# Kernel optimization log

Hardware: AMD Instinct MI355X
Metric: run time of the kernel (lower is better)

The kernel has to match this reference:

```python
import jax, jax.numpy as jnp
import numpy as np

B, N, DIM, H = 4, 2048, 1024, 8
HD = DIM // H
SCALE = HD ** -0.5


def setup_inputs() -> dict:
    key = jax.random.key(0)
    ks = jax.random.split(key, 9)
    inp = {
        "q": jax.random.normal(ks[0], (B, N, DIM), dtype=jnp.float32),
        "k": jax.random.normal(ks[1], (B, N, DIM), dtype=jnp.float32),
        "v": jax.random.normal(ks[2], (B, N, DIM), dtype=jnp.float32),
        "trans_mat": jax.random.normal(ks[3], (B, N, N), dtype=jnp.float32),
        # torch Linear weights: [out_features, in_features]; qkv_bias=False
        "Wq": jax.random.normal(ks[4], (DIM, DIM), dtype=jnp.float32) * (DIM ** -0.5),
        "Wk": jax.random.normal(ks[5], (DIM, DIM), dtype=jnp.float32) * (DIM ** -0.5),
        "Wv": jax.random.normal(ks[6], (DIM, DIM), dtype=jnp.float32) * (DIM ** -0.5),
        "Wp": jax.random.normal(ks[7], (DIM, DIM), dtype=jnp.float32) * (DIM ** -0.5),
        "bp": jax.random.normal(ks[8], (DIM,), dtype=jnp.float32) * 0.01,
    }
    return inp


def reference(q, k, v, trans_mat, Wq, Wk, Wv, Wp, bp):
    Bq, Nq, C = q.shape
    # project and split heads: [B, H, N, HD]
    qh = (q @ Wq.T).reshape(Bq, Nq, H, HD).transpose(0, 2, 1, 3)
    kh = (k @ Wk.T).reshape(Bq, -1, H, HD).transpose(0, 2, 1, 3)
    vh = (v @ Wv.T).reshape(Bq, -1, H, HD).transpose(0, 2, 1, 3)
    # scaled scores gated elementwise by trans_mat (broadcast over heads)
    scores = jnp.einsum("bhqd,bhkd->bhqk", qh, kh) * SCALE
    gated = scores * trans_mat[:, None, :, :]
    # softmax over full row, then zero out positions where gated == 0
    sm = jax.nn.softmax(gated, axis=-1)
    attn = jnp.where(gated != 0, sm, jnp.zeros((), dtype=sm.dtype))
    x = jnp.einsum("bhqk,bhkd->bhqd", attn, vh)
    x = x.transpose(0, 2, 1, 3).reshape(Bq, Nq, C)
    return x @ Wp.T + bp
```

## Files before the change

### kernel.cpp

```cpp
#include <hip/hip_runtime.h>
#include <hip/hip_bf16.h>
#include <stdint.h>

#define B_    4
#define N_    2048
#define DIM_  1024
#define H_    8
#define HD_   128
#define MTOK  (B_ * N_)
#define SCALE_  0.08838834764831845f
#define LOG2E_  1.4426950408889634f
#define QSCALE_ (SCALE_ * LOG2E_)

typedef unsigned short u16;
typedef __attribute__((ext_vector_type(4)))  float f32x4;
typedef __attribute__((ext_vector_type(16))) float f32x16;
typedef __attribute__((ext_vector_type(8)))  short s16x8;
typedef __attribute__((ext_vector_type(8)))  u16  u16x8;
typedef __attribute__((ext_vector_type(4)))  u16  u16x4;
typedef __attribute__((ext_vector_type(4)))  unsigned u32x4;

__device__ __forceinline__ u16 f2bf(float f) {
    uint32_t i = __builtin_bit_cast(uint32_t, f);
    return (u16)((i + 0x7FFFu + ((i >> 16) & 1u)) >> 16);
}
__device__ __forceinline__ unsigned pk_bf16(float a, float b) {
    unsigned r;
    asm("v_cvt_pk_bf16_f32 %0, %1, %2" : "=v"(r) : "v"(a), "v"(b));
    return r;
}
__device__ __forceinline__ void pl32_swap(unsigned &a, unsigned &b) {
    asm volatile("v_permlane32_swap_b32 %0, %1" : "+v"(a), "+v"(b));
}
__device__ __forceinline__ void gl_lds16(const u16* g, u16* l) {
    __builtin_amdgcn_global_load_lds((const __attribute__((address_space(1))) void*)g,
                                     (__attribute__((address_space(3))) void*)l,
                                     16, 0, 0);
}

__global__ __launch_bounds__(256) void cvt_f32_bf16(const float* __restrict__ src,
                                                    u16* __restrict__ dst, int n) {
    int i = (blockIdx.x * 256 + threadIdx.x) * 4;
    int stride = gridDim.x * 256 * 4;
    for (; i < n; i += stride) {
        float4 v = *(const float4*)(src + i);
        u16x4 o;
        o.x = f2bf(v.x); o.y = f2bf(v.y); o.z = f2bf(v.z); o.w = f2bf(v.w);
        *(u16x4*)(dst + i) = o;
    }
}

__global__ __launch_bounds__(256) void cvt_w4(const float* __restrict__ s0,
                                              const float* __restrict__ s1,
                                              const float* __restrict__ s2,
                                              const float* __restrict__ s3,
                                              u16* __restrict__ dst) {
    const float* s = blockIdx.y == 0 ? s0 : blockIdx.y == 1 ? s1 : blockIdx.y == 2 ? s2 : s3;
    u16* d = dst + (size_t)blockIdx.y * (DIM_ * DIM_);
    int i = (blockIdx.x * 256 + threadIdx.x) * 8;
    float4 a = *(const float4*)(s + i);
    float4 b = *(const float4*)(s + i + 4);
    u32x4 w = {pk_bf16(a.x, a.y), pk_bf16(a.z, a.w), pk_bf16(b.x, b.y), pk_bf16(b.z, b.w)};
    *(u16x8*)(d + i) = __builtin_bit_cast(u16x8, w);
}

__global__ __launch_bounds__(256) void transpose_f32(const float* __restrict__ in,
                                                     float* __restrict__ out) {
    __shared__ float t[64][65];
    const int r0 = blockIdx.y * 64, c0 = blockIdx.x * 64;
    const float* ib = in + (size_t)blockIdx.z * N_ * N_;
    float* ob = out + (size_t)blockIdx.z * N_ * N_;
    const int lr = threadIdx.x >> 6, lc = threadIdx.x & 63;
    #pragma unroll
    for (int i = 0; i < 16; i++)
        t[i * 4 + lr][lc] = ib[(size_t)(r0 + i * 4 + lr) * N_ + c0 + lc];
    __syncthreads();
    #pragma unroll
    for (int i = 0; i < 16; i++)
        ob[(size_t)(c0 + i * 4 + lr) * N_ + r0 + lc] = t[lc][i * 4 + lr];
}

template <int MODE>
__global__ __launch_bounds__(256) void gemm_bt(const u16* __restrict__ A,
                                               const u16* __restrict__ Bt,
                                               void* __restrict__ Cout,
                                               const float* __restrict__ bias,
                                               float scale, int M, int NN, int K) {
    __shared__ __align__(16) u16 lga[128 * 64];
    __shared__ __align__(16) u16 lgb[128 * 64];
    const int tid  = threadIdx.x;
    const int lane = tid & 63, wave = tid >> 6;
    const int wm = wave >> 1, wn = wave & 1;
    const int row0 = blockIdx.y * 128, col0 = blockIdx.x * 128;

    f32x4 acc[4][4] = {};

    auto stageLds = [&](const u16* G, u16* L, int rowbase, int k0) {
        #pragma unroll
        for (int i = 0; i < 4; i++) {
            int rb = wave * 32 + i * 8;
            int r  = rb + (lane >> 3);
            int cc = (lane & 7) ^ (lane >> 3);
            gl_lds16(G + (size_t)(rowbase + r) * K + k0 + cc * 8, L + rb * 64);
        }
    };

    for (int k0 = 0; k0 < K; k0 += 64) {
        stageLds(A,  lga, row0, k0);
        stageLds(Bt, lgb, col0, k0);
        __syncthreads();
        #pragma unroll
        for (int kk = 0; kk < 2; kk++) {
            s16x8 af[4], bfr[4];
            #pragma unroll
            for (int mi = 0; mi < 4; mi++) {
                int r = wm * 64 + mi * 16 + (lane & 15);
                int sc = (kk * 4 + (lane >> 4)) ^ (lane & 7);
                af[mi] = *(const s16x8*)(&lga[r * 64 + sc * 8]);
            }
            #pragma unroll
            for (int ni = 0; ni < 4; ni++) {
                int r = wn * 64 + ni * 16 + (lane & 15);
                int sc = (kk * 4 + (lane >> 4)) ^ (lane & 7);
                bfr[ni] = *(const s16x8*)(&lgb[r * 64 + sc * 8]);
            }
            #pragma unroll
            for (int mi = 0; mi < 4; mi++)
                #pragma unroll
                for (int ni = 0; ni < 4; ni++)
                    acc[mi][ni] = __builtin_amdgcn_mfma_f32_16x16x32_bf16(
                        af[mi], bfr[ni], acc[mi][ni], 0, 0, 0);
        }
        __syncthreads();
    }

    #pragma unroll
    for (int mi = 0; mi < 4; mi++) {
        #pragma unroll
        for (int ni = 0; ni < 4; ni++) {
            #pragma unroll
            for (int r = 0; r < 4; r++) {
                int grow = row0 + wm * 64 + mi * 16 + ((lane >> 4) << 2) + r;
                int gcol = col0 + wn * 64 + ni * 16 + (lane & 15);
                float vv = acc[mi][ni][r];
                if (MODE == 2) {
                    ((float*)Cout)[(size_t)grow * NN + gcol] = vv + bias[gcol];
                } else {
                    vv *= scale;
                    int bb = grow >> 11, n = grow & (N_ - 1);
                    int hh = gcol >> 7,  d = gcol & (HD_ - 1);
                    size_t idx = (MODE == 0)
                        ? ((size_t)(bb * H_ + hh) * N_ + n) * HD_ + d
                        : ((size_t)(bb * H_ + hh) * HD_ + d) * N_ + n;
                    ((u16*)Cout)[idx] = f2bf(vv);
                }
            }
        }
    }
}

__global__ __launch_bounds__(256, 2) void attn_swapped(const u16* __restrict__ Qh,
                                                       const u16* __restrict__ Kh,
                                                       const u16* __restrict__ Vt,
                                                       const float* __restrict__ transT,
                                                       u16* __restrict__ xout) {
    __shared__ __align__(16) u16 kt[2][64 * 128];
    __shared__ __align__(16) u16 vt[2][128 * 64];

    const int tid = threadIdx.x, lane = tid & 63, wave = tid >> 6;
    const int lq = lane & 31, hl = lane >> 5;

    int lin = blockIdx.x + 16 * (blockIdx.y + 8 * blockIdx.z);
    int nl  = (lin & 7) * 64 + (lin >> 3);
    const int qt = nl & 15, hh = (nl >> 4) & 7, b = nl >> 7;
    const int q0 = qt * 128 + wave * 32;
    const int q  = q0 + lq;

    const u16* Qbh = Qh + (size_t)(b * H_ + hh) * N_ * HD_;
    const u16* Kbh = Kh + (size_t)(b * H_ + hh) * N_ * HD_;
    const u16* Vbh = Vt + (size_t)(b * H_ + hh) * HD_ * N_;
    const float* tTq = transT + (size_t)b * N_ * N_ + q;

    s16x8 qf[8];
    #pragma unroll
    for (int s = 0; s < 8; s++)
        qf[s] = *(const s16x8*)(Qbh + (size_t)q * HD_ + s * 16 + hl * 8);

    auto stageKV = [&](int kv0, int bi) {
        #pragma unroll
        for (int i = 0; i < 4; i++) {
            int rk = wave * 16 + i * 4 + (lane >> 4);
            int ck = (lane & 15) ^ (rk & 15) ^ ((rk & 16) >> 2);
            gl_lds16(Kbh + (size_t)(kv0 + rk) * HD_ + ck * 8,
                     &kt[bi][(wave * 16 + i * 4) * 128]);
            int rv = wave * 32 + i * 8 + (lane >> 3);
            int cv = (lane & 7) ^ (rv & 7) ^ ((rv >> 3) & 3);
            gl_lds16(Vbh + (size_t)rv * N_ + kv0 + cv * 8,
                     &vt[bi][(wave * 32 + i * 8) * 64]);
        }
    };

    const int mKl = (lq & 15) ^ ((lq & 16) >> 2);
    const int mVl = (lq & 7) ^ ((lq >> 3) & 3);

    float m = -3.0e38f, l = 0.f;
    f32x16 aoT[4] = {};

    stageKV(0, 0);
    __syncthreads();

    for (int it = 0; it < N_ / 64; it++) {
        const int kv0 = it * 64, cur = it & 1;
        if (it + 1 < N_ / 64) stageKV(kv0 + 64, cur ^ 1);

        float tt[2][16];
        #pragma unroll
        for (int ni = 0; ni < 2; ni++)
            #pragma unroll
            for (int idx = 0; idx < 16; idx++) {
                int kv = (idx & 3) + 8 * (idx >> 2) + 4 * hl + 32 * ni;
                tt[ni][idx] = tTq[(size_t)(kv0 + kv) * N_];
            }

        f32x16 sT[2] = {};
        __builtin_amdgcn_s_setprio(1);
        #pragma unroll
        for (int s = 0; s < 8; s++)
            #pragma unroll
            for (int ni = 0; ni < 2; ni++) {
                int r = ni * 32 + lq;
                int slot = (2 * s + hl) ^ mKl;
                s16x8 kf = *(const s16x8*)(&kt[cur][r * 128 + slot * 8]);
                sT[ni] = __builtin_amdgcn_mfma_f32_32x32x16_bf16(kf, qf[s], sT[ni], 0, 0, 0);
            }
        __builtin_amdgcn_s_setprio(0);

        float mx = -3.0e38f;
        #pragma unroll
        for (int ni = 0; ni < 2; ni++)
            #pragma unroll
            for (int idx = 0; idx < 16; idx++) {
                float g = sT[ni][idx] * tt[ni][idx];
                sT[ni][idx] = g;
                mx = fmaxf(mx, g);
            }
        mx = fmaxf(mx, __shfl_xor(mx, 32));

        if (__any(mx > m + 8.0f)) {
            float mn = fmaxf(m, mx);
            float sfv = __builtin_amdgcn_exp2f(m - mn);
            m = mn;
            l *= sfv;
            #pragma unroll
            for (int dt = 0; dt < 4; dt++)
                #pragma unroll
                for (int e = 0; e < 16; e++) aoT[dt][e] *= sfv;
        }

        float rs = 0.f;
        #pragma unroll
        for (int ni = 0; ni < 2; ni++)
            #pragma unroll
            for (int e = 0; e < 16; e++) {
                float g = sT[ni][e];
                float p = __builtin_amdgcn_exp2f(g - m);
                rs += p;
                sT[ni][e] = (g != 0.0f) ? p : 0.0f;
            }
        rs += __shfl_xor(rs, 32);
        l += rs;

        s16x8 pfrag[4];
        #pragma unroll
        for (int sp = 0; sp < 4; sp++) {
            const int ni = sp >> 1;
            const int ru = (2 * sp) & 3, rv2 = (2 * sp + 1) & 3;
            unsigned u0 = pk_bf16(sT[ni][ru * 4 + 0], sT[ni][ru * 4 + 1]);
            unsigned u1 = pk_bf16(sT[ni][ru * 4 + 2], sT[ni][ru * 4 + 3]);
            unsigned v0 = pk_bf16(sT[ni][rv2 * 4 + 0], sT[ni][rv2 * 4 + 1]);
            unsigned v1 = pk_bf16(sT[ni][rv2 * 4 + 2], sT[ni][rv2 * 4 + 3]);
            pl32_swap(u0, v0);
            pl32_swap(u1, v1);
            u32x4 w = {u0, u1, v0, v1};
            pfrag[sp] = __builtin_bit_cast(s16x8, w);
        }

        __builtin_amdgcn_s_setprio(1);
        #pragma unroll
        for (int dt = 0; dt < 4; dt++)
            #pragma unroll
            for (int sp = 0; sp < 4; sp++) {
                int r = dt * 32 + lq;
                int slot = (2 * sp + hl) ^ mVl;
                s16x8 vf = *(const s16x8*)(&vt[cur][r * 64 + slot * 8]);
                aoT[dt] = __builtin_amdgcn_mfma_f32_32x32x16_bf16(vf, pfrag[sp], aoT[dt], 0, 0, 0);
            }
        __builtin_amdgcn_s_setprio(0);
        __syncthreads();
    }

    float inv = 1.0f / l;
    u16* orow = xout + ((size_t)(b * N_ + q)) * DIM_ + hh * HD_;
    #pragma unroll
    for (int dt = 0; dt < 4; dt++)
        #pragma unroll
        for (int r2 = 0; r2 < 4; r2++) {
            u16x4 ov;
            #pragma unroll
            for (int e = 0; e < 4; e++)
                ov[e] = f2bf(aoT[dt][r2 * 4 + e] * inv);
            *(u16x4*)(orow + dt * 32 + r2 * 8 + hl * 4) = ov;
        }
}

__global__ __launch_bounds__(512) void attn_fb(const u16* __restrict__ Qh,
                                               const u16* __restrict__ Kh,
                                               const u16* __restrict__ Vt,
                                               const float* __restrict__ trans,
                                               u16* __restrict__ xout) {
    __shared__ __align__(16) u16 kt[64 * 128];
    __shared__ __align__(16) u16 vt[128 * 64];
    __shared__ __align__(16) u16 plds[8][16 * 72];

    const int tid = threadIdx.x, lane = tid & 63, wave = tid >> 6;
    const int qt = blockIdx.x, h = blockIdx.y, b = blockIdx.z;
    const int qrow_base = qt * 128 + wave * 16;

    const u16* Qbh = Qh + (size_t)(b * H_ + h) * N_ * HD_;
    const u16* Kbh = Kh + (size_t)(b * H_ + h) * N_ * HD_;
    const u16* Vbh = Vt + (size_t)(b * H_ + h) * HD_ * N_;
    const float* trow = trans + (size_t)b * N_ * N_
                      + (size_t)(qrow_base + ((lane >> 4) << 2)) * N_ + (lane & 15);

    s16x8 qf[4];
    {
        int r = qrow_base + (lane & 15);
        #pragma unroll
        for (int kd = 0; kd < 4; kd++)
            qf[kd] = *(const s16x8*)(Qbh + (size_t)r * HD_ + kd * 32 + ((lane >> 4) << 3));
    }
    auto stageKV = [&](int kv0) {
        int rbk = wave * 8, rbv = wave * 16;
        #pragma unroll
        for (int j = 0; j < 2; j++) {
            int c = j * 64 + lane;
            int rk = rbk + (c >> 4), ck = (c & 15) ^ (rk & 15);
            gl_lds16(Kbh + (size_t)(kv0 + rk) * HD_ + ck * 8, kt + rbk * 128 + j * 512);
            int rv = rbv + (c >> 3), cv = (c & 7) ^ (rv & 7);
            gl_lds16(Vbh + (size_t)rv * N_ + kv0 + cv * 8, vt + rbv * 64 + j * 512);
        }
    };

    float m[4], l[4];
    #pragma unroll
    for (int r = 0; r < 4; r++) { m[r] = -3.0e38f; l[r] = 0.f; }
    f32x4 ao[8] = {};

    for (int kv0 = 0; kv0 < N_; kv0 += 64) {
        stageKV(kv0);
        __syncthreads();
        f32x4 s[4] = {};
        #pragma unroll
        for (int kd = 0; kd < 4; kd++)
            #pragma unroll
            for (int ni = 0; ni < 4; ni++) {
                int r = ni * 16 + (lane & 15);
                int sc = (kd * 4 + (lane >> 4)) ^ (lane & 15);
                s16x8 bfr = *(const s16x8*)(&kt[r * 128 + sc * 8]);
                s[ni] = __builtin_amdgcn_mfma_f32_16x16x32_bf16(qf[kd], bfr, s[ni], 0, 0, 0);
            }
        float pmax[4] = {-3.0e38f, -3.0e38f, -3.0e38f, -3.0e38f};
        #pragma unroll
        for (int ni = 0; ni < 4; ni++)
            #pragma unroll
            for (int r = 0; r < 4; r++) {
                float tt = trow[(size_t)r * N_ + kv0 + ni * 16];
                float gg = s[ni][r] * tt;
                s[ni][r] = gg;
                pmax[r] = fmaxf(pmax[r], gg);
            }
        #pragma unroll
        for (int r = 0; r < 4; r++) {
            float p = pmax[r];
            p = fmaxf(p, __shfl_xor(p, 1));
            p = fmaxf(p, __shfl_xor(p, 2));
            p = fmaxf(p, __shfl_xor(p, 4));
            p = fmaxf(p, __shfl_xor(p, 8));
            pmax[r] = p;
        }
        bool need = false;
        #pragma unroll
        for (int r = 0; r < 4; r++) need = need || (pmax[r] > m[r] + 8.0f);
        if (__any(need)) {
            #pragma unroll
            for (int r = 0; r < 4; r++) {
                float mn = fmaxf(m[r], pmax[r]);
                float sfv = __builtin_amdgcn_exp2f(m[r] - mn);
                m[r] = mn; l[r] *= sfv;
                #pragma unroll
                for (int t = 0; t < 8; t++) ao[t][r] *= sfv;
            }
        }
        float rowsum[4] = {0.f, 0.f, 0.f, 0.f};
        u16* pw = &plds[wave][0];
        #pragma unroll
        for (int ni = 0; ni < 4; ni++)
            #pragma unroll
            for (int r = 0; r < 4; r++) {
                float gg = s[ni][r];
                float e = __builtin_amdgcn_exp2f(gg - m[r]);
                rowsum[r] += e;
                float pe = (gg != 0.0f) ? e : 0.0f;
                pw[(((lane >> 4) << 2) + r) * 72 + ni * 16 + (lane & 15)] = f2bf(pe);
            }
        #pragma unroll
        for (int r = 0; r < 4; r++) {
            float ssum = rowsum[r];
            ssum += __shfl_xor(ssum, 1);
            ssum += __shfl_xor(ssum, 2);
            ssum += __shfl_xor(ssum, 4);
            ssum += __shfl_xor(ssum, 8);
            l[r] += ssum;
        }
        #pragma unroll
        for (int kk = 0; kk < 2; kk++) {
            s16x8 pa = *(const s16x8*)(&pw[(lane & 15) * 72 + kk * 32 + ((lane >> 4) << 3)]);
            #pragma unroll
            for (int t = 0; t < 8; t++) {
                int r = t * 16 + (lane & 15);
                int sc = (kk * 4 + (lane >> 4)) ^ (r & 7);
                s16x8 vb = *(const s16x8*)(&vt[r * 64 + sc * 8]);
                ao[t] = __builtin_amdgcn_mfma_f32_16x16x32_bf16(pa, vb, ao[t], 0, 0, 0);
            }
        }
        __syncthreads();
    }
    #pragma unroll
    for (int r = 0; r < 4; r++) {
        float inv = 1.0f / l[r];
        int n = qrow_base + ((lane >> 4) << 2) + r;
        u16* orow = xout + ((size_t)(b * N_ + n)) * DIM_ + h * HD_;
        #pragma unroll
        for (int t = 0; t < 8; t++)
            orow[t * 16 + (lane & 15)] = f2bf(ao[t][r] * inv);
    }
}

extern "C" void kernel_launch(void* const* d_in, const int* in_sizes, int n_in,
                              void* d_out, int out_size, void* d_ws, size_t ws_size,
                              hipStream_t stream) {
    const float* q     = (const float*)d_in[0];
    const float* k     = (const float*)d_in[1];
    const float* v     = (const float*)d_in[2];
    const float* trans = (const float*)d_in[3];
    const float* Wq    = (const float*)d_in[4];
    const float* Wk    = (const float*)d_in[5];
    const float* Wv    = (const float*)d_in[6];
    const float* Wp    = (const float*)d_in[7];
    const float* bp    = (const float*)d_in[8];

    char* ws = (char*)d_ws;
    u16* tmp = (u16*)(ws);
    u16* wqb = (u16*)(ws + (16u << 20));
    u16* wkb = (u16*)(ws + (18u << 20));
    u16* wvb = (u16*)(ws + (20u << 20));
    u16* wpb = (u16*)(ws + (22u << 20));
    u16* QhB = (u16*)(ws + (24u << 20));
    u16* KhB = (u16*)(ws + (40u << 20));
    u16* VtB = (u16*)(ws + (56u << 20));
    float* tT = (float*)(ws + (72u << 20));
    u16* xb  = tmp;
    const bool big = ws_size >= (136ull << 20);

    dim3 blk(256);
    cvt_w4<<<dim3(512, 4), blk, 0, stream>>>(Wq, Wk, Wv, Wp, wqb);

    dim3 pg(DIM_ / 128, MTOK / 128);

    cvt_f32_bf16<<<dim3(8192), blk, 0, stream>>>(q, tmp, MTOK * DIM_);
    gemm_bt<0><<<pg, blk, 0, stream>>>(tmp, wqb, QhB, nullptr, QSCALE_, MTOK, DIM_, DIM_);
    cvt_f32_bf16<<<dim3(8192), blk, 0, stream>>>(k, tmp, MTOK * DIM_);
    gemm_bt<0><<<pg, blk, 0, stream>>>(tmp, wkb, KhB, nullptr, 1.0f, MTOK, DIM_, DIM_);
    cvt_f32_bf16<<<dim3(8192), blk, 0, stream>>>(v, tmp, MTOK * DIM_);
    gemm_bt<1><<<pg, blk, 0, stream>>>(tmp, wvb, VtB, nullptr, 1.0f, MTOK, DIM_, DIM_);

    if (big) {
        transpose_f32<<<dim3(N_ / 64, N_ / 64, B_), blk, 0, stream>>>(trans, tT);
        attn_swapped<<<dim3(16, 8, 4), dim3(256), 0, stream>>>(QhB, KhB, VtB, tT, xb);
    } else {
        attn_fb<<<dim3(N_ / 128, H_, B_), dim3(512), 0, stream>>>(QhB, KhB, VtB, trans, xb);
    }

    gemm_bt<2><<<pg, blk, 0, stream>>>(xb, wpb, d_out, bp, 1.0f, MTOK, DIM_, DIM_);
}
```

Before: 276.2 us.

## Software-pipeline attention PV with next QK, vectorize transpose, swizzle GEMM blocks

The attention loop is restructured so each iteration's P·V MFMAs (using the previous tile's probabilities) are issued between the QK^T score computation and the softmax of the current tile. V goes to a triple-buffered LDS ring to support this, and the P fragments ping-pong between two register sets. The aim is to overlap matrix-core work with the softmax VALU work. The trans_mat transpose now uses float4 global loads and stores, and the GEMM remaps block indices for better L2 locality. Risks are higher register and LDS pressure (80KB LDS per block), which could hurt the two-blocks-per-CU occupancy target. The GEMM remap also hardcodes an 8-column, 512-block grid.

```diff
diff --git a/kernel.cpp b/kernel.cpp
--- a/kernel.cpp
+++ b/kernel.cpp
@@ -70,14 +70,24 @@
     const int r0 = blockIdx.y * 64, c0 = blockIdx.x * 64;
     const float* ib = in + (size_t)blockIdx.z * N_ * N_;
     float* ob = out + (size_t)blockIdx.z * N_ * N_;
-    const int lr = threadIdx.x >> 6, lc = threadIdx.x & 63;
-    #pragma unroll
-    for (int i = 0; i < 16; i++)
-        t[i * 4 + lr][lc] = ib[(size_t)(r0 + i * 4 + lr) * N_ + c0 + lc];
+    const int lr = threadIdx.x >> 4;
+    const int lc = threadIdx.x & 15;
+    #pragma unroll
+    for (int i = 0; i < 4; i++) {
+        int row = i * 16 + lr;
+        float4 v = *(const float4*)(ib + (size_t)(r0 + row) * N_ + c0 + lc * 4);
+        t[row][lc * 4 + 0] = v.x; t[row][lc * 4 + 1] = v.y;
+        t[row][lc * 4 + 2] = v.z; t[row][lc * 4 + 3] = v.w;
+    }
     __syncthreads();
     #pragma unroll
-    for (int i = 0; i < 16; i++)
-        ob[(size_t)(c0 + i * 4 + lr) * N_ + r0 + lc] = t[lc][i * 4 + lr];
+    for (int i = 0; i < 4; i++) {
+        int row = i * 16 + lr;
+        float4 w;
+        w.x = t[lc * 4 + 0][row]; w.y = t[lc * 4 + 1][row];
+        w.z = t[lc * 4 + 2][row]; w.w = t[lc * 4 + 3][row];
+        *(float4*)(ob + (size_t)(c0 + row) * N_ + r0 + lc * 4) = w;
+    }
 }
 
 template <int MODE>
@@ -91,7 +101,9 @@
     const int tid  = threadIdx.x;
     const int lane = tid & 63, wave = tid >> 6;
     const int wm = wave >> 1, wn = wave & 1;
-    const int row0 = blockIdx.y * 128, col0 = blockIdx.x * 128;
+    int lin = blockIdx.x + gridDim.x * blockIdx.y;
+    int w   = (lin & 7) * 64 + (lin >> 3);
+    const int row0 = (w >> 3) * 128, col0 = (w & 7) * 128;
 
     f32x4 acc[4][4] = {};
 
@@ -165,7 +177,7 @@
                                                        const float* __restrict__ transT,
                                                        u16* __restrict__ xout) {
     __shared__ __align__(16) u16 kt[2][64 * 128];
-    __shared__ __align__(16) u16 vt[2][128 * 64];
+    __shared__ __align__(16) u16 vt[3][128 * 64];
 
     const int tid = threadIdx.x, lane = tid & 63, wave = tid >> 6;
     const int lq = lane & 31, hl = lane >> 5;
@@ -186,17 +198,17 @@
     for (int s = 0; s < 8; s++)
         qf[s] = *(const s16x8*)(Qbh + (size_t)q * HD_ + s * 16 + hl * 8);
 
-    auto stageKV = [&](int kv0, int bi) {
+    auto stageKV = [&](int kv0, int kbi, int vbi) {
         #pragma unroll
         for (int i = 0; i < 4; i++) {
             int rk = wave * 16 + i * 4 + (lane >> 4);
             int ck = (lane & 15) ^ (rk & 15) ^ ((rk & 16) >> 2);
             gl_lds16(Kbh + (size_t)(kv0 + rk) * HD_ + ck * 8,
-                     &kt[bi][(wave * 16 + i * 4) * 128]);
+                     &kt[kbi][(wave * 16 + i * 4) * 128]);
             int rv = wave * 32 + i * 8 + (lane >> 3);
             int cv = (lane & 7) ^ (rv & 7) ^ ((rv >> 3) & 3);
             gl_lds16(Vbh + (size_t)rv * N_ + kv0 + cv * 8,
-                     &vt[bi][(wave * 32 + i * 8) * 64]);
+                     &vt[vbi][(wave * 32 + i * 8) * 64]);
         }
     };
 
@@ -205,13 +217,16 @@
 
     float m = -3.0e38f, l = 0.f;
     f32x16 aoT[4] = {};
-
-    stageKV(0, 0);
+    s16x8 pfA[4], pfB[4];
+    int kc = 0, vc = 0, vprev = 2;
+
+    stageKV(0, 0, 0);
     __syncthreads();
 
-    for (int it = 0; it < N_ / 64; it++) {
-        const int kv0 = it * 64, cur = it & 1;
-        if (it + 1 < N_ / 64) stageKV(kv0 + 64, cur ^ 1);
+    auto body = [&](int it, s16x8 (&pprev)[4], s16x8 (&pcur)[4], bool doPV) {
+        const int kv0 = it * 64;
+        const int vnext = (vc == 2) ? 0 : vc + 1;
+        if (it + 1 < N_ / 64) stageKV(kv0 + 64, kc ^ 1, vnext);
 
         float tt[2][16];
         #pragma unroll
@@ -230,7 +245,7 @@
             for (int ni = 0; ni < 2; ni++) {
                 int r = ni * 32 + lq;
                 int slot = (2 * s + hl) ^ mKl;
-                s16x8 kf = *(const s16x8*)(&kt[cur][r * 128 + slot * 8]);
+                s16x8 kf = *(const s16x8*)(&kt[kc][r * 128 + slot * 8]);
                 sT[ni] = __builtin_amdgcn_mfma_f32_32x32x16_bf16(kf, qf[s], sT[ni], 0, 0, 0);
             }
         __builtin_amdgcn_s_setprio(0);
@@ -245,6 +260,18 @@
                 mx = fmaxf(mx, g);
             }
         mx = fmaxf(mx, __shfl_xor(mx, 32));
+
+        if (doPV) {
+            #pragma unroll
+            for (int dt = 0; dt < 4; dt++)
+                #pragma unroll
+                for (int sp = 0; sp < 4; sp++) {
+                    int r = dt * 32 + lq;
+                    int slot = (2 * sp + hl) ^ mVl;
+                    s16x8 vf = *(const s16x8*)(&vt[vprev][r * 64 + slot * 8]);
+                    aoT[dt] = __builtin_amdgcn_mfma_f32_32x32x16_bf16(vf, pprev[sp], aoT[dt], 0, 0, 0);
+                }
+        }
 
         if (__any(mx > m + 8.0f)) {
             float mn = fmaxf(m, mx);
@@ -270,7 +297,6 @@
         rs += __shfl_xor(rs, 32);
         l += rs;
 
-        s16x8 pfrag[4];
         #pragma unroll
         for (int sp = 0; sp < 4; sp++) {
             const int ni = sp >> 1;
@@ -282,22 +308,30 @@
             pl32_swap(u0, v0);
             pl32_swap(u1, v1);
             u32x4 w = {u0, u1, v0, v1};
-            pfrag[sp] = __builtin_bit_cast(s16x8, w);
-        }
-
-        __builtin_amdgcn_s_setprio(1);
-        #pragma unroll
-        for (int dt = 0; dt < 4; dt++)
-            #pragma unroll
-            for (int sp = 0; sp < 4; sp++) {
-                int r = dt * 32 + lq;
-                int slot = (2 * sp + hl) ^ mVl;
-                s16x8 vf = *(const s16x8*)(&vt[cur][r * 64 + slot * 8]);
-                aoT[dt] = __builtin_amdgcn_mfma_f32_32x32x16_bf16(vf, pfrag[sp], aoT[dt], 0, 0, 0);
-            }
-        __builtin_amdgcn_s_setprio(0);
+            pcur[sp] = __builtin_bit_cast(s16x8, w);
+        }
+
+        vprev = vc; vc = vnext; kc ^= 1;
         __syncthreads();
-    }
+    };
+
+    body(0, pfA, pfA, false);
+    #pragma unroll 1
+    for (int j = 0; j < 15; j++) {
+        body(2 * j + 1, pfA, pfB, true);
+        body(2 * j + 2, pfB, pfA, true);
+    }
+    body(31, pfA, pfB, true);
+
+    #pragma unroll
+    for (int dt = 0; dt < 4; dt++)
+        #pragma unroll
+        for (int sp = 0; sp < 4; sp++) {
+            int r = dt * 32 + lq;
+            int slot = (2 * sp + hl) ^ mVl;
+            s16x8 vf = *(const s16x8*)(&vt[vprev][r * 64 + slot * 8]);
+            aoT[dt] = __builtin_amdgcn_mfma_f32_32x32x16_bf16(vf, pfB[sp], aoT[dt], 0, 0, 0);
+        }
 
     float inv = 1.0f / l;
     u16* orow = xout + ((size_t)(b * N_ + q)) * DIM_ + hh * HD_;
```

Result: slower. 294.3 us (+6.5%).
